# Performance work log

Measured on AMD Instinct MI355X. Metric: run time of the kernel, lower is better.

The kernel has to match this reference:

```python
import jax, jax.numpy as jnp
import numpy as np

RES = 0.1


def setup_inputs() -> dict:
    key = jax.random.key(0)
    k1, k2 = jax.random.split(key)
    B, N, H, W = 512, 8192, 200, 200
    # positions in [-11, 11] so some points land out of the valid [-9.9, 9.9] range
    opState = jax.random.uniform(k1, (B, N, 2), dtype=jnp.float32, minval=-11.0, maxval=11.0)
    # ESDF distances in [0, 2) meters
    envs = jax.random.uniform(k2, (B, 1, H, W), dtype=jnp.float32) * 2.0
    return {"opState": opState, "envs": envs}


def reference(opState, envs):
    # opState: [B, N, 2] world positions; envs: [B, 1, 200, 200] ESDF map
    out_range = jnp.any((opState < -9.9) | (opState > 9.9), axis=-1)  # [B, N]
    pos = jnp.clip(opState, -9.9, 9.9)
    pos_m = pos - 0.5 * RES
    idx = jnp.floor((pos_m + 10.0) / RES).astype(jnp.int32)           # [B, N, 2]
    idx_pos = (idx.astype(jnp.float32) + 0.5) * RES - 10.0
    diff = (pos - idx_pos) / RES                                       # [B, N, 2]

    esdf = envs[:, 0]                                                  # [B, H, W]
    b = jnp.arange(esdf.shape[0])[:, None]                             # [B, 1]
    ix, iy = idx[..., 0], idx[..., 1]
    # 4-corner gather for bilinear interpolation
    v00 = esdf[b, ix,     iy    ]
    v10 = esdf[b, ix + 1, iy    ]
    v01 = esdf[b, ix,     iy + 1]
    v11 = esdf[b, ix + 1, iy + 1]

    dx, dy = diff[..., 0], diff[..., 1]
    vx0 = (1.0 - dx) * v00 + dx * v10
    vx1 = (1.0 - dx) * v01 + dx * v11
    v = (1.0 - dy) * vx0 + dy * vx1
    dists = jnp.where(out_range, -1.0, v)                              # [B, N]

    viod = 10.0 * (0.3 - dists)
    penalty = jnp.square(jax.nn.relu(viod))  # positiveSmoothedL2
    return jnp.mean(penalty)
```

## Files before the change

kernel.cpp:

```cpp
#include <hip/hip_runtime.h>
#include <hip/hip_bf16.h>

#define RES 0.1f

constexpr int B_ = 512;
constexpr int N_ = 8192;
constexpr int H_ = 200;
constexpr int W_ = 200;
constexpr int MAP = H_ * W_;
constexpr long long TOTAL = (long long)B_ * N_;

constexpr int TPB = 1024;
constexpr int PPT = 8;
constexpr int V4  = PPT / 2;
constexpr int BATCH = 4;

__global__ __launch_bounds__(TPB, 8) void collision_lds(
    const float* __restrict__ opState,
    const float* __restrict__ envs,
    float* __restrict__ partial)
{
    __shared__ __hip_bfloat16 smap[MAP + 4];
    const int b   = blockIdx.x;
    const int tid = threadIdx.x;

    const float4* pts4 = (const float4*)((const float2*)opState + (long long)b * N_);
    float4 p[V4];
    #pragma unroll
    for (int k = 0; k < V4; ++k)
        p[k] = pts4[tid + k * TPB];

    {
        const float4* m4 = (const float4*)(envs + (long long)b * MAP);
        ushort4* s4 = (ushort4*)smap;
        #pragma unroll
        for (int j = 0; j < 10; ++j) {
            int idx = tid + j * TPB;
            if (idx < MAP / 4) {
                float4 m = m4[idx];
                __hip_bfloat16 h0 = __float2bfloat16(m.x);
                __hip_bfloat16 h1 = __float2bfloat16(m.y);
                __hip_bfloat16 h2 = __float2bfloat16(m.z);
                __hip_bfloat16 h3 = __float2bfloat16(m.w);
                ushort4 u;
                u.x = *(const unsigned short*)&h0;
                u.y = *(const unsigned short*)&h1;
                u.z = *(const unsigned short*)&h2;
                u.w = *(const unsigned short*)&h3;
                s4[idx] = u;
            }
        }
    }
    __syncthreads();

    const unsigned int* smapw = (const unsigned int*)smap;
    float acc = 0.0f;

    #pragma unroll
    for (int bat = 0; bat < PPT / BATCH; ++bat) {
        int   jr0[BATCH];
        int   jr1[BATCH];
        int   sel[BATCH];
        float dxA[BATCH], dyA[BATCH];
        bool  orA[BATCH];

        #pragma unroll
        for (int t = 0; t < BATCH; ++t) {
            const int pt = bat * BATCH + t;
            const float4 pv = p[pt >> 1];
            const float qx = (pt & 1) ? pv.z : pv.x;
            const float qy = (pt & 1) ? pv.w : pv.y;

            orA[t] = (qx < -9.9f) | (qx > 9.9f) | (qy < -9.9f) | (qy > 9.9f);

            float px = fminf(fmaxf(qx, -9.9f), 9.9f);
            float py = fminf(fmaxf(qy, -9.9f), 9.9f);

            float pmx = px - 0.5f * RES;
            float pmy = py - 0.5f * RES;

            int ix = (int)floorf((pmx + 10.0f) * 10.0f);
            int iy = (int)floorf((pmy + 10.0f) * 10.0f);

            float ipx = ((float)ix + 0.5f) * RES - 10.0f;
            float ipy = ((float)iy + 0.5f) * RES - 10.0f;

            dxA[t] = (px - ipx) * 10.0f;
            dyA[t] = (py - ipy) * 10.0f;

            const int base = ix * W_ + iy;
            jr0[t] = base >> 1;
            jr1[t] = (base + W_) >> 1;
            sel[t] = base & 1;
        }

        unsigned int w00[BATCH], w01[BATCH], w10[BATCH], w11[BATCH];
        #pragma unroll
        for (int t = 0; t < BATCH; ++t) {
            w00[t] = smapw[jr0[t]];
            w01[t] = smapw[jr0[t] + 1];
            w10[t] = smapw[jr1[t]];
            w11[t] = smapw[jr1[t] + 1];
        }

        #pragma unroll
        for (int t = 0; t < BATCH; ++t) {
            unsigned int c00 = sel[t] ? (w00[t] >> 16)      : (w00[t] & 0xffffu);
            unsigned int c01 = sel[t] ? (w01[t] & 0xffffu)  : (w00[t] >> 16);
            unsigned int c10 = sel[t] ? (w10[t] >> 16)      : (w10[t] & 0xffffu);
            unsigned int c11 = sel[t] ? (w11[t] & 0xffffu)  : (w10[t] >> 16);

            c00 <<= 16; c01 <<= 16; c10 <<= 16; c11 <<= 16;
            float v00 = __uint_as_float(c00);
            float v01 = __uint_as_float(c01);
            float v10 = __uint_as_float(c10);
            float v11 = __uint_as_float(c11);

            float dx = dxA[t], dy = dyA[t];
            float vx0 = (1.0f - dx) * v00 + dx * v10;
            float vx1 = (1.0f - dx) * v01 + dx * v11;
            float v   = (1.0f - dy) * vx0 + dy * vx1;

            float dists = orA[t] ? -1.0f : v;
            float viod  = 10.0f * (0.3f - dists);
            float r     = viod > 0.0f ? viod : 0.0f;
            acc += r * r;
        }
    }

    #pragma unroll
    for (int off = 32; off > 0; off >>= 1)
        acc += __shfl_down(acc, off, 64);

    __shared__ float sacc[TPB / 64];
    const int lane = tid & 63;
    const int wid  = tid >> 6;
    if (lane == 0) sacc[wid] = acc;
    __syncthreads();

    if (tid == 0) {
        float s = 0.0f;
        #pragma unroll
        for (int w = 0; w < TPB / 64; ++w) s += sacc[w];
        partial[b] = s;
    }
}

__global__ __launch_bounds__(512) void collision_final(
    const float* __restrict__ partial,
    float* __restrict__ out)
{
    float acc = partial[threadIdx.x];

    #pragma unroll
    for (int off = 32; off > 0; off >>= 1)
        acc += __shfl_down(acc, off, 64);

    __shared__ float sacc[8];
    const int lane = threadIdx.x & 63;
    const int wid  = threadIdx.x >> 6;
    if (lane == 0) sacc[wid] = acc;
    __syncthreads();

    if (threadIdx.x == 0) {
        float s = 0.0f;
        #pragma unroll
        for (int w = 0; w < 8; ++w) s += sacc[w];
        out[0] = s / (float)TOTAL;
    }
}

extern "C" void kernel_launch(void* const* d_in, const int* in_sizes, int n_in,
                              void* d_out, int out_size, void* d_ws, size_t ws_size,
                              hipStream_t stream) {
    const float* opState = (const float*)d_in[0];
    const float* envs    = (const float*)d_in[1];
    float* out     = (float*)d_out;
    float* partial = (float*)d_ws;

    collision_lds<<<B_, TPB, 0, stream>>>(opState, envs, partial);
    collision_final<<<1, 512, 0, stream>>>(partial, out);
}
```

Measured before the change: 146.8 us.

## Process two batches per block, prefetching second map during first compute

Halves the grid so each block handles two batch elements. The second ESDF map and its points are loaded into registers while the first batch is interpolated from LDS, then converted into a second LDS buffer. This aims to hide global-load latency inside a block, at the cost of double LDS use per block, which limits occupancy to one block per CU and adds register pressure.

```diff
diff --git a/kernel.cpp b/kernel.cpp
--- a/kernel.cpp
+++ b/kernel.cpp
@@ -8,59 +8,23 @@
 constexpr int H_ = 200;
 constexpr int W_ = 200;
 constexpr int MAP = H_ * W_;
+constexpr int MAPW = MAP / 2;
 constexpr long long TOTAL = (long long)B_ * N_;
 
-constexpr int TPB = 1024;
-constexpr int PPT = 8;
-constexpr int V4  = PPT / 2;
+constexpr int NBLK = 256;
+constexpr int TPB  = 1024;
+constexpr int PPT  = 8;
+constexpr int V4   = PPT / 2;
+constexpr int MV4  = 10;
 constexpr int BATCH = 4;
 
-__global__ __launch_bounds__(TPB, 8) void collision_lds(
-    const float* __restrict__ opState,
-    const float* __restrict__ envs,
-    float* __restrict__ partial)
-{
-    __shared__ __hip_bfloat16 smap[MAP + 4];
-    const int b   = blockIdx.x;
-    const int tid = threadIdx.x;
-
-    const float4* pts4 = (const float4*)((const float2*)opState + (long long)b * N_);
-    float4 p[V4];
-    #pragma unroll
-    for (int k = 0; k < V4; ++k)
-        p[k] = pts4[tid + k * TPB];
-
-    {
-        const float4* m4 = (const float4*)(envs + (long long)b * MAP);
-        ushort4* s4 = (ushort4*)smap;
-        #pragma unroll
-        for (int j = 0; j < 10; ++j) {
-            int idx = tid + j * TPB;
-            if (idx < MAP / 4) {
-                float4 m = m4[idx];
-                __hip_bfloat16 h0 = __float2bfloat16(m.x);
-                __hip_bfloat16 h1 = __float2bfloat16(m.y);
-                __hip_bfloat16 h2 = __float2bfloat16(m.z);
-                __hip_bfloat16 h3 = __float2bfloat16(m.w);
-                ushort4 u;
-                u.x = *(const unsigned short*)&h0;
-                u.y = *(const unsigned short*)&h1;
-                u.z = *(const unsigned short*)&h2;
-                u.w = *(const unsigned short*)&h3;
-                s4[idx] = u;
-            }
-        }
-    }
-    __syncthreads();
-
-    const unsigned int* smapw = (const unsigned int*)smap;
+__device__ __forceinline__ float compute_batch(const float4 p[V4],
+                                               const unsigned int* __restrict__ smapw)
+{
     float acc = 0.0f;
-
     #pragma unroll
     for (int bat = 0; bat < PPT / BATCH; ++bat) {
-        int   jr0[BATCH];
-        int   jr1[BATCH];
-        int   sel[BATCH];
+        int   jr0[BATCH], jr1[BATCH], sel[BATCH];
         float dxA[BATCH], dyA[BATCH];
         bool  orA[BATCH];
 
@@ -105,16 +69,15 @@
 
         #pragma unroll
         for (int t = 0; t < BATCH; ++t) {
-            unsigned int c00 = sel[t] ? (w00[t] >> 16)      : (w00[t] & 0xffffu);
-            unsigned int c01 = sel[t] ? (w01[t] & 0xffffu)  : (w00[t] >> 16);
-            unsigned int c10 = sel[t] ? (w10[t] >> 16)      : (w10[t] & 0xffffu);
-            unsigned int c11 = sel[t] ? (w11[t] & 0xffffu)  : (w10[t] >> 16);
-
-            c00 <<= 16; c01 <<= 16; c10 <<= 16; c11 <<= 16;
-            float v00 = __uint_as_float(c00);
-            float v01 = __uint_as_float(c01);
-            float v10 = __uint_as_float(c10);
-            float v11 = __uint_as_float(c11);
+            unsigned int c00 = sel[t] ? (w00[t] >> 16)     : (w00[t] & 0xffffu);
+            unsigned int c01 = sel[t] ? (w01[t] & 0xffffu) : (w00[t] >> 16);
+            unsigned int c10 = sel[t] ? (w10[t] >> 16)     : (w10[t] & 0xffffu);
+            unsigned int c11 = sel[t] ? (w11[t] & 0xffffu) : (w10[t] >> 16);
+
+            float v00 = __uint_as_float(c00 << 16);
+            float v01 = __uint_as_float(c01 << 16);
+            float v10 = __uint_as_float(c10 << 16);
+            float v11 = __uint_as_float(c11 << 16);
 
             float dx = dxA[t], dy = dyA[t];
             float vx0 = (1.0f - dx) * v00 + dx * v10;
@@ -127,6 +90,74 @@
             acc += r * r;
         }
     }
+    return acc;
+}
+
+__device__ __forceinline__ uint2 cvt4(float4 m)
+{
+    __hip_bfloat16 h0 = __float2bfloat16(m.x);
+    __hip_bfloat16 h1 = __float2bfloat16(m.y);
+    __hip_bfloat16 h2 = __float2bfloat16(m.z);
+    __hip_bfloat16 h3 = __float2bfloat16(m.w);
+    unsigned int lo = (unsigned int)*(const unsigned short*)&h0 |
+                      ((unsigned int)*(const unsigned short*)&h1 << 16);
+    unsigned int hi = (unsigned int)*(const unsigned short*)&h2 |
+                      ((unsigned int)*(const unsigned short*)&h3 << 16);
+    return make_uint2(lo, hi);
+}
+
+__global__ __launch_bounds__(TPB, 4) void collision_pipe(
+    const float* __restrict__ opState,
+    const float* __restrict__ envs,
+    float* __restrict__ partial)
+{
+    __shared__ uint2 bufA[MAPW / 2 + 1];
+    __shared__ uint2 bufB[MAPW / 2 + 1];
+
+    const int bid = blockIdx.x;
+    const int tid = threadIdx.x;
+    const int b0 = bid;
+    const int b1 = bid + NBLK;
+
+    const float4* pts0 = (const float4*)((const float2*)opState + (long long)b0 * N_);
+    float4 p0[V4];
+    #pragma unroll
+    for (int k = 0; k < V4; ++k)
+        p0[k] = pts0[tid + k * TPB];
+
+    {
+        const float4* m4 = (const float4*)(envs + (long long)b0 * MAP);
+        #pragma unroll
+        for (int j = 0; j < MV4; ++j) {
+            int idx = tid + j * TPB;
+            if (idx < MAP / 4) bufA[idx] = cvt4(m4[idx]);
+        }
+    }
+    __syncthreads();
+
+    const float4* m4b = (const float4*)(envs + (long long)b1 * MAP);
+    float4 mreg[MV4];
+    #pragma unroll
+    for (int j = 0; j < MV4; ++j) {
+        int idx = tid + j * TPB;
+        mreg[j] = (idx < MAP / 4) ? m4b[idx] : make_float4(0.f, 0.f, 0.f, 0.f);
+    }
+    const float4* pts1 = (const float4*)((const float2*)opState + (long long)b1 * N_);
+    float4 p1[V4];
+    #pragma unroll
+    for (int k = 0; k < V4; ++k)
+        p1[k] = pts1[tid + k * TPB];
+
+    float acc = compute_batch(p0, (const unsigned int*)bufA);
+
+    #pragma unroll
+    for (int j = 0; j < MV4; ++j) {
+        int idx = tid + j * TPB;
+        if (idx < MAP / 4) bufB[idx] = cvt4(mreg[j]);
+    }
+    __syncthreads();
+
+    acc += compute_batch(p1, (const unsigned int*)bufB);
 
     #pragma unroll
     for (int off = 32; off > 0; off >>= 1)
@@ -142,11 +173,11 @@
         float s = 0.0f;
         #pragma unroll
         for (int w = 0; w < TPB / 64; ++w) s += sacc[w];
-        partial[b] = s;
-    }
-}
-
-__global__ __launch_bounds__(512) void collision_final(
+        partial[bid] = s;
+    }
+}
+
+__global__ __launch_bounds__(256) void collision_final(
     const float* __restrict__ partial,
     float* __restrict__ out)
 {
@@ -156,16 +187,14 @@
     for (int off = 32; off > 0; off >>= 1)
         acc += __shfl_down(acc, off, 64);
 
-    __shared__ float sacc[8];
+    __shared__ float sacc[4];
     const int lane = threadIdx.x & 63;
     const int wid  = threadIdx.x >> 6;
     if (lane == 0) sacc[wid] = acc;
     __syncthreads();
 
     if (threadIdx.x == 0) {
-        float s = 0.0f;
-        #pragma unroll
-        for (int w = 0; w < 8; ++w) s += sacc[w];
+        float s = sacc[0] + sacc[1] + sacc[2] + sacc[3];
         out[0] = s / (float)TOTAL;
     }
 }
@@ -178,6 +207,6 @@
     float* out     = (float*)d_out;
     float* partial = (float*)d_ws;
 
-    collision_lds<<<B_, TPB, 0, stream>>>(opState, envs, partial);
-    collision_final<<<1, 512, 0, stream>>>(partial, out);
-}
+    collision_pipe<<<NBLK, TPB, 0, stream>>>(opState, envs, partial);
+    collision_final<<<1, 256, 0, stream>>>(partial, out);
+}
```

After: 148.7 us. No clear change (+1.3%).
